# Performance work log

Measured on AMD Instinct MI355X. Metric: run time of the kernel, lower is better.

## Reference

```python
import jax, jax.numpy as jnp
import numpy as np

C = 256      # embed_dim
GROUP = 2    # conv groups
K = 3        # kernel/pool size
K2 = K * K
OG = 8       # offset groups (hard-coded in Similarity_cal)
NEX = 3      # exemplars per image (out_conv expects group*3*4 channels)


def conv2d(x, w, b, pad):
    y = jax.lax.conv_general_dilated(x, w, (1, 1), [(pad, pad), (pad, pad)],
                                     dimension_numbers=("NCHW", "OIHW", "NCHW"))
    return y + b[None, :, None, None]


def ln_c(x, g, b, eps=1e-5):
    # LayerNorm over the channel axis of NCHW (torch permutes to NHWC, LN, permute back)
    mu = x.mean(axis=1, keepdims=True)
    var = ((x - mu) ** 2).mean(axis=1, keepdims=True)
    return (x - mu) / jnp.sqrt(var + eps) * g[None, :, None, None] + b[None, :, None, None]


def bilinear_gather(img, py, px):
    # img [Cg,H,W]; py,px [K2,H,W] -> samples [Cg,K2,H,W], zero outside borders
    Cg, H, W = img.shape
    y0f = jnp.floor(py); x0f = jnp.floor(px)
    wy = py - y0f; wx = px - x0f
    y0 = y0f.astype(jnp.int32); x0 = x0f.astype(jnp.int32)
    flat = img.reshape(Cg, H * W)

    def corner(yy, xx, w):
        valid = (yy >= 0) & (yy < H) & (xx >= 0) & (xx < W)
        idx = jnp.clip(yy, 0, H - 1) * W + jnp.clip(xx, 0, W - 1)
        v = jnp.take(flat, idx.reshape(-1), axis=1).reshape(Cg, K2, H, W)
        return v * (w * valid)[None]

    return (corner(y0, x0, (1 - wy) * (1 - wx)) + corner(y0, x0 + 1, (1 - wy) * wx)
            + corner(y0 + 1, x0, wy * (1 - wx)) + corner(y0 + 1, x0 + 1, wy * wx))


def deform_conv(x, offset, mask, weight, dilation):
    # x [C,H,W]; offset [2*OG*K2,H,W]; mask [OG*K2,H,W] (softmaxed); weight [NEX*GROUP, C//GROUP, K, K]
    Cc, H, W = x.shape
    pad = (K - 1) * dilation // 2
    off = offset.reshape(OG, K2, 2, H, W)  # (dy, dx) per offset-group / tap
    kk = jnp.arange(K, dtype=x.dtype)
    ky = jnp.repeat(kk, K) * dilation - pad  # [K2]
    kx = jnp.tile(kk, K) * dilation - pad
    ii = jnp.arange(H, dtype=x.dtype)
    jj = jnp.arange(W, dtype=x.dtype)
    py = ii[None, None, :, None] + ky[None, :, None, None] + off[:, :, 0]  # [OG,K2,H,W]
    px = jj[None, None, None, :] + kx[None, :, None, None] + off[:, :, 1]
    xg = x.reshape(OG, Cc // OG, H, W)
    samp = jax.vmap(bilinear_gather)(xg, py, px)              # [OG,Cg,K2,H,W]
    samp = samp * mask.reshape(OG, 1, K2, H, W)               # modulation
    samp = samp.reshape(GROUP, Cc // GROUP, K2, H, W)
    wR = weight.reshape(NEX * GROUP, Cc // GROUP, K2)
    gidx = jnp.arange(NEX * GROUP) // NEX                     # out-channel -> conv group
    return jnp.einsum("rck,rckhw->rhw", wR, samp[gidx])       # [NEX*GROUP,H,W]


def forward(querys_feat, supports_feat, in_w, in_b, ln_g, ln_b, out_w, out_b,
            offw1, offb1, mskw1, mskb1, offw2, offb2, mskw2, mskb2,
            offw4, offb4, mskw4, mskb4):
    B = querys_feat.shape[0]
    q = ln_c(conv2d(querys_feat, in_w, in_b, 0), ln_g, ln_b)                 # [B,C,H,W]
    s = supports_feat.reshape(B * NEX, C, K, K)
    s = ln_c(conv2d(s, in_w, in_b, 0), ln_g, ln_b).reshape(B, NEX, C, K, K)

    def offs(wo, bo, wm, bm):
        o = conv2d(q, wo, bo, (K - 1) // 2)
        m = jax.nn.softmax(conv2d(q, wm, bm, (K - 1) // 2), axis=1)  # softmax over all OG*K2 channels
        return o, m

    o1, m1 = offs(offw1, offb1, mskw1, mskb1)
    o2, m2 = offs(offw2, offb2, mskw2, mskb2)
    o4, m4 = offs(offw4, offb4, mskw4, mskb4)

    def per_sample(qi, si, o1i, m1i, o2i, m2i, o4i, m4i):
        w = si.reshape(NEX * GROUP, C // GROUP, K, K)         # dynamic per-exemplar kernels
        pooled = si.max(axis=(2, 3)).reshape(NEX * GROUP, C // GROUP)
        gidx = jnp.arange(NEX * GROUP) // NEX
        qg = qi.reshape(GROUP, C // GROUP, *qi.shape[1:])
        sim0 = jnp.einsum("rc,rchw->rhw", pooled, qg[gidx])   # grouped 1x1 conv branch
        d1 = deform_conv(qi, o1i, m1i, w, 1)
        d2 = deform_conv(qi, o2i, m2i, w, 2)
        d4 = deform_conv(qi, o4i, m4i, w, 4)
        return jnp.concatenate([sim0, d1, d2, d4], axis=0)    # [GROUP*3*4, H, W]

    sim = jax.vmap(per_sample)(q, s, o1, m1, o2, m2, o4, m4)
    return conv2d(sim, out_w, out_b, 0)                        # [B,C,H,W]


def setup_inputs() -> dict:
    key = jax.random.key(0)
    ks = jax.random.split(key, 20)
    B, H, W = 2, 96, 96
    inp = {
        "querys_feat": jax.random.normal(ks[0], (B, C, H, W), jnp.float32),
        "supports_feat": jax.random.normal(ks[1], (B, NEX, C, K, K), jnp.float32),
        "in_w": jax.random.normal(ks[2], (C, C, 1, 1), jnp.float32) / 16.0,
        "in_b": jax.random.normal(ks[3], (C,), jnp.float32) * 0.02,
        "ln_g": jnp.ones((C,), jnp.float32),
        "ln_b": jnp.zeros((C,), jnp.float32),
        "out_w": jax.random.normal(ks[4], (C, GROUP * 3 * 4, 1, 1), jnp.float32) * 0.2,
        "out_b": jax.random.normal(ks[5], (C,), jnp.float32) * 0.02,
    }
    i = 6
    for d in (1, 2, 4):
        inp[f"offw{d}"] = jax.random.normal(ks[i], (2 * OG * K2, C, K, K), jnp.float32) * 0.01; i += 1
        inp[f"offb{d}"] = jax.random.normal(ks[i], (2 * OG * K2,), jnp.float32) * 0.1; i += 1
        inp[f"mskw{d}"] = jax.random.normal(ks[i], (OG * K2, C, K, K), jnp.float32) * 0.02; i += 1
        inp[f"mskb{d}"] = jax.random.normal(ks[i], (OG * K2,), jnp.float32) * 0.1; i += 1
    return inp


def reference(querys_feat, supports_feat, in_w, in_b, ln_g, ln_b, out_w, out_b,
              offw1, offb1, mskw1, mskb1, offw2, offb2, mskw2, mskb2,
              offw4, offb4, mskw4, mskb4):
    return forward(querys_feat, supports_feat, in_w, in_b, ln_g, ln_b, out_w, out_b,
                   offw1, offb1, mskw1, mskb1, offw2, offb2, mskw2, mskb2,
                   offw4, offb4, mskw4, mskb4)
```

## Files before the change

kernel.cpp:

```cpp
#include <hip/hip_runtime.h>
#include <hip/hip_bf16.h>
#include <math.h>

#define HH 96
#define WWID 96
#define HW 9216
#define CC 256
#define BB 2
#define PROW 104
#define PCOL 128
#define PPX (PROW * PCOL)

typedef float f32x4 __attribute__((ext_vector_type(4)));
typedef _Float16 f16x8 __attribute__((ext_vector_type(8)));
typedef _Float16 h2v __attribute__((ext_vector_type(2)));

__device__ inline unsigned int pack2h(float a, float b) {
  unsigned short ua = __builtin_bit_cast(unsigned short, (_Float16)a);
  unsigned short ub = __builtin_bit_cast(unsigned short, (_Float16)b);
  return (unsigned int)ua | ((unsigned int)ub << 16);
}

#if defined(__has_builtin)
#if __has_builtin(__builtin_amdgcn_fdot2)
#define FDOT2(a, b, c) __builtin_amdgcn_fdot2((a), (b), (c), false)
#endif
#endif
#ifndef FDOT2
#define FDOT2(a, b, c) ((c) + (float)(a).x * (float)(b).x + (float)(a).y * (float)(b).y)
#endif

__device__ inline void gload_lds16(const void* g, void* l) {
  __builtin_amdgcn_global_load_lds(
      (const __attribute__((address_space(1))) void*)g,
      (__attribute__((address_space(3))) void*)l, 16, 0, 0);
}

__global__ void k_transpose_w(const float* __restrict__ in_w, float* __restrict__ wT) {
  int k = blockIdx.x, c = threadIdx.x;
  wT[k * CC + c] = in_w[c * CC + k];
}

__global__ void k_packw(const float* __restrict__ ow1, const float* __restrict__ ob1,
                        const float* __restrict__ mw1, const float* __restrict__ mb1,
                        const float* __restrict__ ow2, const float* __restrict__ ob2,
                        const float* __restrict__ mw2, const float* __restrict__ mb2,
                        const float* __restrict__ ow4, const float* __restrict__ ob4,
                        const float* __restrict__ mw4, const float* __restrict__ mb4,
                        _Float16* __restrict__ Whf, float* __restrict__ Ball) {
  int idx = blockIdx.x * 256 + threadIdx.x;
  if (idx >= 3 * 256 * 2304) return;
  int d = idx / (256 * 2304);
  int rem = idx - d * 256 * 2304;
  int co = rem / 2304;
  int k = rem - co * 2304;
  int j = k >> 8, ci = k & 255;
  const float* ow = d == 0 ? ow1 : (d == 1 ? ow2 : ow4);
  const float* mw = d == 0 ? mw1 : (d == 1 ? mw2 : mw4);
  float v = 0.f;
  if (co < 144) v = ow[co * 2304 + ci * 9 + j];
  else if (co < 216) v = mw[(co - 144) * 2304 + ci * 9 + j];
  Whf[idx] = (_Float16)v;
  if (idx < 768) {
    int dd = idx >> 8, cc = idx & 255;
    const float* obv = dd == 0 ? ob1 : (dd == 1 ? ob2 : ob4);
    const float* mbv = dd == 0 ? mb1 : (dd == 1 ? mb2 : mb4);
    float bv = 0.f;
    if (cc < 144) bv = obv[cc];
    else if (cc < 216) bv = mbv[cc - 144];
    Ball[idx] = bv;
  }
}

__global__ void k_conv1_ln_q(const float* __restrict__ qin, const float* __restrict__ wT,
                             const float* __restrict__ in_b, const float* __restrict__ ln_g,
                             const float* __restrict__ ln_b, float* __restrict__ q_hwc,
                             _Float16* __restrict__ qpad) {
  int bx = blockIdx.x;
  int b = bx / 288;
  int hw0 = (bx % 288) * 32;
  int t = threadIdx.x;
  int lane = t & 63;
  int wv_id = t >> 6;
  __shared__ float xs[32 * 260];
  const float* qb = qin + (size_t)b * CC * HW;
  #pragma unroll
  for (int i = 0; i < 32; ++i) {
    int idx = t + i * 256;
    int p = idx & 31;
    int k = idx >> 5;
    xs[p * 260 + k] = qb[k * HW + hw0 + p];
  }
  __syncthreads();
  float acc[8][4];
  #pragma unroll
  for (int p = 0; p < 8; ++p) { acc[p][0]=0.f; acc[p][1]=0.f; acc[p][2]=0.f; acc[p][3]=0.f; }
  const float4* wT4 = (const float4*)wT;
  int p0 = wv_id * 8;
  for (int k = 0; k < 256; k += 4) {
    float4 w0 = wT4[(k + 0) * 64 + lane];
    float4 w1 = wT4[(k + 1) * 64 + lane];
    float4 w2 = wT4[(k + 2) * 64 + lane];
    float4 w3 = wT4[(k + 3) * 64 + lane];
    #pragma unroll
    for (int p = 0; p < 8; ++p) {
      float4 xv = *(const float4*)&xs[(p0 + p) * 260 + k];
      acc[p][0] += w0.x * xv.x + w1.x * xv.y + w2.x * xv.z + w3.x * xv.w;
      acc[p][1] += w0.y * xv.x + w1.y * xv.y + w2.y * xv.z + w3.y * xv.w;
      acc[p][2] += w0.z * xv.x + w1.z * xv.y + w2.z * xv.z + w3.z * xv.w;
      acc[p][3] += w0.w * xv.x + w1.w * xv.y + w2.w * xv.z + w3.w * xv.w;
    }
  }
  float4 bb = ((const float4*)in_b)[lane];
  float4 g4 = ((const float4*)ln_g)[lane];
  float4 b4 = ((const float4*)ln_b)[lane];
  #pragma unroll
  for (int p = 0; p < 8; ++p) {
    float y0 = acc[p][0] + bb.x, y1 = acc[p][1] + bb.y;
    float y2 = acc[p][2] + bb.z, y3 = acc[p][3] + bb.w;
    float s1 = y0 + y1 + y2 + y3;
    float s2 = y0*y0 + y1*y1 + y2*y2 + y3*y3;
    #pragma unroll
    for (int off = 32; off; off >>= 1) { s1 += __shfl_xor(s1, off); s2 += __shfl_xor(s2, off); }
    float mu = s1 * (1.f / 256.f);
    float rstd = rsqrtf(s2 * (1.f / 256.f) - mu * mu + 1e-5f);
    float4 o;
    o.x = (y0 - mu) * rstd * g4.x + b4.x;
    o.y = (y1 - mu) * rstd * g4.y + b4.y;
    o.z = (y2 - mu) * rstd * g4.z + b4.z;
    o.w = (y3 - mu) * rstd * g4.w + b4.w;
    int hw = hw0 + p0 + p;
    ((float4*)q_hwc)[((size_t)b * HW + hw) * 64 + lane] = o;
    int hh = hw / 96, ww = hw - hh * 96;
    int ppx = (hh + 4) * PCOL + ww + 4;
    struct alignas(8) h4 { _Float16 h[4]; };
    h4 oh;
    oh.h[0] = (_Float16)o.x; oh.h[1] = (_Float16)o.y;
    oh.h[2] = (_Float16)o.z; oh.h[3] = (_Float16)o.w;
    *(h4*)(qpad + ((size_t)b * PPX + ppx) * CC + lane * 4) = oh;
  }
}

__global__ void k_conv1_ln_s(const float* __restrict__ sup, const float* __restrict__ wT,
                             const float* __restrict__ in_b, const float* __restrict__ ln_g,
                             const float* __restrict__ ln_b, float* __restrict__ s_ln,
                             float* __restrict__ pooled) {
  int img = blockIdx.x;
  int t = threadIdx.x;
  __shared__ float xs[2304];
  __shared__ float red1[256], red2[256];
  #pragma unroll
  for (int p = 0; p < 9; ++p) xs[t * 9 + p] = sup[(size_t)img * 2304 + t * 9 + p];
  __syncthreads();
  float acc[9];
  #pragma unroll
  for (int p = 0; p < 9; ++p) acc[p] = 0.f;
  for (int k = 0; k < 256; ++k) {
    float wv = wT[k * CC + t];
    #pragma unroll
    for (int p = 0; p < 9; ++p) acc[p] += wv * xs[k * 9 + p];
  }
  float bias = in_b[t];
  #pragma unroll
  for (int p = 0; p < 9; ++p) acc[p] += bias;
  float g = ln_g[t], be = ln_b[t];
  float vals[9];
  #pragma unroll
  for (int p = 0; p < 9; ++p) {
    red1[t] = acc[p]; red2[t] = acc[p] * acc[p];
    __syncthreads();
    for (int s = 128; s > 0; s >>= 1) {
      if (t < s) { red1[t] += red1[t + s]; red2[t] += red2[t + s]; }
      __syncthreads();
    }
    float mu = red1[0] * (1.f / 256.f);
    float var = red2[0] * (1.f / 256.f) - mu * mu;
    float rstd = rsqrtf(var + 1e-5f);
    vals[p] = (acc[p] - mu) * rstd * g + be;
    __syncthreads();
  }
  #pragma unroll
  for (int p = 0; p < 9; ++p) s_ln[(size_t)img * 2304 + t * 9 + p] = vals[p];
  float mx = vals[0];
  #pragma unroll
  for (int p = 1; p < 9; ++p) mx = fmaxf(mx, vals[p]);
  int b = img / 3, e = img % 3;
  pooled[((size_t)b * 6 + e * 2 + (t >> 7)) * 128 + (t & 127)] = mx;
}


#define BAR() __builtin_amdgcn_s_barrier()
#define SCHEDB() __builtin_amdgcn_sched_barrier(0)
#define VMCNT(N) asm volatile("s_waitcnt vmcnt(" #N ")" ::: "memory")

#define MMA_ONE(M, N, S, QM, QN) \
  acc[(QM)*4+(M)][(QN)*2+(N)] = __builtin_amdgcn_mfma_f32_16x16x32_f16( \
      af[M][S], bf[(QN)*2+(N)][S], acc[(QM)*4+(M)][(QN)*2+(N)], 0, 0, 0);

#define MMA_Q(QM, QN) { \
  __builtin_amdgcn_s_setprio(1); \
  MMA_ONE(0,0,0,QM,QN) MMA_ONE(1,0,0,QM,QN) MMA_ONE(2,0,0,QM,QN) MMA_ONE(3,0,0,QM,QN) \
  MMA_ONE(0,1,0,QM,QN) MMA_ONE(1,1,0,QM,QN) MMA_ONE(2,1,0,QM,QN) MMA_ONE(3,1,0,QM,QN) \
  MMA_ONE(0,0,1,QM,QN) MMA_ONE(1,0,1,QM,QN) MMA_ONE(2,0,1,QM,QN) MMA_ONE(3,0,1,QM,QN) \
  MMA_ONE(0,1,1,QM,QN) MMA_ONE(1,1,1,QM,QN) MMA_ONE(2,1,1,QM,QN) MMA_ONE(3,1,1,QM,QN) \
  __builtin_amdgcn_s_setprio(0); }

#define LDA(BUF, QM) { \
  const char* p_ = smemB + (BUF) * 65536 + (wm * 128 + (QM) * 64 + l15) * 128; \
  af[0][0] = *(const f16x8*)(p_ + 0*2048 + rc0); af[0][1] = *(const f16x8*)(p_ + 0*2048 + rc1); \
  af[1][0] = *(const f16x8*)(p_ + 1*2048 + rc0); af[1][1] = *(const f16x8*)(p_ + 1*2048 + rc1); \
  af[2][0] = *(const f16x8*)(p_ + 2*2048 + rc0); af[2][1] = *(const f16x8*)(p_ + 2*2048 + rc1); \
  af[3][0] = *(const f16x8*)(p_ + 3*2048 + rc0); af[3][1] = *(const f16x8*)(p_ + 3*2048 + rc1); }

#define LDB(BUF, QN) { \
  const char* p_ = smemB + (BUF) * 65536 + 32768 + (wn * 64 + (QN) * 32 + l15) * 128; \
  bf[(QN)*2+0][0] = *(const f16x8*)(p_ + 0*2048 + rc0); bf[(QN)*2+0][1] = *(const f16x8*)(p_ + 0*2048 + rc1); \
  bf[(QN)*2+1][0] = *(const f16x8*)(p_ + 1*2048 + rc0); bf[(QN)*2+1][1] = *(const f16x8*)(p_ + 1*2048 + rc1); }

#define STAGEA(TILE, Q) { \
  gload_lds16(aBase + (size_t)((Q) * 64) * 2304 + (TILE) * 64, \
              smemB + ((TILE) & 1) * 65536 + (((Q) * 64 + wv * 8) * 128)); \
  gload_lds16(aBase + (size_t)(128 + (Q) * 64) * 2304 + (TILE) * 64, \
              smemB + ((TILE) & 1) * 65536 + ((128 + (Q) * 64 + wv * 8) * 128)); }

#define STAGEB(TILE, Q, PPX0, PPX1) { \
  int j_ = (TILE) >> 2; \
  int offp_ = (j_ / 3 - 1) * PCOL + (j_ % 3) - 1; \
  int cb_ = ((TILE) & 3) * 64; \
  int rs_ = (wv >> 2) * 64 + (Q) * 32 + (wv & 3) * 8; \
  gload_lds16(bBase + (size_t)((PPX0) + offp_) * CC + cb_, \
              smemB + ((TILE) & 1) * 65536 + 32768 + (rs_ * 128)); \
  gload_lds16(bBase + (size_t)((PPX1) + offp_) * CC + cb_, \
              smemB + ((TILE) & 1) * 65536 + 32768 + ((128 + rs_) * 128)); }

__global__ void __launch_bounds__(512) k_conv3_mfma8(
    const _Float16* __restrict__ qpad, const _Float16* __restrict__ Whf,
    const float* __restrict__ Ball, unsigned int* __restrict__ taprec) {
  int nb = blockIdx.x;
  int z = blockIdx.y;
  int d = z >> 1, b = z & 1;
  int t = threadIdx.x;
  int lane = t & 63, wv = t >> 6;
  int wm = wv >> 2, wn = wv & 3;
  int quad = lane >> 4, l15 = lane & 15;
  int l8 = lane >> 3, c7 = lane & 7;

  __shared__ _Float16 __attribute__((aligned(16))) smem[65536];
  char* smemB = (char*)smem;

  const _Float16* Wd = Whf + (size_t)d * 256 * 2304;
  const _Float16* qb = qpad + (size_t)b * PPX * CC;

  int scol = ((c7 ^ l8) << 3);
  int rc0 = ((quad ^ (l15 & 7)) << 4);
  int rc1 = (((4 | quad) ^ (l15 & 7)) << 4);

  const _Float16* aBase = Wd + (size_t)(wv * 8 + l8) * 2304 + scol;
  const _Float16* bBase = qb + scol;

  int ppx00, ppx01, ppx10, ppx11;
  {
    int rbase = (wv >> 2) * 64 + (wv & 3) * 8 + l8;
    int px, hh, ww;
    px = nb * 256 + rbase;             hh = px / 96; ww = px - hh * 96; ppx00 = (hh + 4) * PCOL + ww + 4;
    px = nb * 256 + 128 + rbase;       hh = px / 96; ww = px - hh * 96; ppx01 = (hh + 4) * PCOL + ww + 4;
    px = nb * 256 + 32 + rbase;        hh = px / 96; ww = px - hh * 96; ppx10 = (hh + 4) * PCOL + ww + 4;
    px = nb * 256 + 160 + rbase;       hh = px / 96; ww = px - hh * 96; ppx11 = (hh + 4) * PCOL + ww + 4;
  }

  f32x4 acc[8][4];
  #pragma unroll
  for (int i = 0; i < 8; ++i)
    #pragma unroll
    for (int j = 0; j < 4; ++j) acc[i][j] = (f32x4){0.f, 0.f, 0.f, 0.f};

  f16x8 af[4][2], bf[4][2];

  STAGEA(0, 0);
  STAGEB(0, 1, ppx10, ppx11);
  STAGEA(0, 1);
  STAGEB(0, 0, ppx00, ppx01);
  STAGEA(1, 0);
  STAGEB(1, 1, ppx10, ppx11);
  VMCNT(4);
  BAR();
  SCHEDB();

  #pragma unroll 1
  for (int ii = 0; ii < 17; ++ii) {
    int ta = 2 * ii + 1, tb = 2 * ii + 2, tc = 2 * ii + 3;
    LDA(0, 0) LDB(0, 0)
    STAGEA(ta, 1);
    BAR(); MMA_Q(0, 0); BAR();
    LDB(0, 1)
    STAGEB(ta, 0, ppx00, ppx01);
    BAR(); MMA_Q(0, 1); BAR();
    LDA(0, 1)
    STAGEA(tb, 0);
    BAR(); MMA_Q(1, 1); BAR();
    STAGEB(tb, 1, ppx10, ppx11);
    VMCNT(4);
    BAR(); SCHEDB(); MMA_Q(1, 0); BAR();
    LDA(1, 0) LDB(1, 0)
    STAGEA(tb, 1);
    BAR(); MMA_Q(0, 0); BAR();
    LDB(1, 1)
    STAGEB(tb, 0, ppx00, ppx01);
    BAR(); MMA_Q(0, 1); BAR();
    LDA(1, 1)
    STAGEA(tc, 0);
    BAR(); MMA_Q(1, 1); BAR();
    STAGEB(tc, 1, ppx10, ppx11);
    VMCNT(4);
    BAR(); SCHEDB(); MMA_Q(1, 0); BAR();
  }

  LDA(0, 0) LDB(0, 0)
  STAGEA(35, 1);
  BAR(); MMA_Q(0, 0); BAR();
  LDB(0, 1)
  STAGEB(35, 0, ppx00, ppx01);
  BAR(); MMA_Q(0, 1); BAR();
  LDA(0, 1)
  BAR(); MMA_Q(1, 1); BAR();
  VMCNT(0);
  BAR(); SCHEDB(); MMA_Q(1, 0); BAR();
  LDA(1, 0) LDB(1, 0)
  BAR(); MMA_Q(0, 0); BAR();
  LDB(1, 1)
  BAR(); MMA_Q(0, 1); BAR();
  LDA(1, 1)
  BAR(); MMA_Q(1, 1); BAR();
  MMA_Q(1, 0);

  BAR();
  float* cs = (float*)smemB;
  const float* Bd = Ball + d * 256;
  unsigned int* tzo = taprec + (size_t)z * 72 * HW * 3;
  int sub = t & 7;
  int pxq = t >> 3;
  int dil = 1 << d;

  #pragma unroll 1
  for (int H = 0; H < 2; ++H) {
    if ((wn >> 1) == H) {
      #pragma unroll
      for (int mi = 0; mi < 8; ++mi) {
        int c2 = wm * 128 + mi * 16 + quad * 4;
        if (c2 < 216) {
          float4 bq = *(const float4*)(Bd + c2);
          #pragma unroll
          for (int ni = 0; ni < 4; ++ni) {
            int pl = (wn & 1) * 64 + ni * 16 + l15;
            f32x4 v = acc[mi][ni];
            float* cp = &cs[pl * 225 + c2];
            cp[0] = v[0] + bq.x; cp[1] = v[1] + bq.y;
            cp[2] = v[2] + bq.z; cp[3] = v[3] + bq.w;
          }
        }
      }
    }
    BAR();
    #pragma unroll 1
    for (int p = 0; p < 2; ++p) {
      int pl = p * 64 + pxq;
      int px = nb * 256 + H * 128 + pl;
      const float* cr = &cs[pl * 225];
      float lg[9];
      float mx = -1e30f;
      #pragma unroll
      for (int j = 0; j < 9; ++j) {
        lg[j] = cr[144 + sub + 8 * j];
        mx = fmaxf(mx, lg[j]);
      }
      mx = fmaxf(mx, __shfl_xor(mx, 1));
      mx = fmaxf(mx, __shfl_xor(mx, 2));
      mx = fmaxf(mx, __shfl_xor(mx, 4));
      float s = 0.f;
      #pragma unroll
      for (int j = 0; j < 9; ++j) s += __expf(lg[j] - mx);
      s += __shfl_xor(s, 1);
      s += __shfl_xor(s, 2);
      s += __shfl_xor(s, 4);
      float rinv = 1.f / s;
      int h = px / WWID, w = px - h * WWID;
      int k = sub;
      #pragma unroll
      for (int j = 0; j < 9; ++j) {
        int tk = sub + 8 * j;
        float dy = cr[tk * 2 + 0];
        float dx = cr[tk * 2 + 1];
        float m = __expf(lg[j] - mx) * rinv;
        float py = (float)(h + (k / 3) * dil - dil) + dy;
        float pxx = (float)(w + (k % 3) * dil - dil) + dx;
        float y0f = floorf(py), x0f = floorf(pxx);
        int y0 = (int)y0f, x0 = (int)x0f;
        float wy = py - y0f, wx = pxx - x0f;
        bool vy0 = (unsigned)y0 < 96u, vy1 = (unsigned)(y0 + 1) < 96u;
        bool vx0 = (unsigned)x0 < 96u, vx1 = (unsigned)(x0 + 1) < 96u;
        float w00 = (vy0 && vx0) ? (1.f - wy) * (1.f - wx) * m : 0.f;
        float w01 = (vy0 && vx1) ? (1.f - wy) * wx * m : 0.f;
        float w10 = (vy1 && vx0) ? wy * (1.f - wx) * m : 0.f;
        float w11 = (vy1 && vx1) ? wy * wx * m : 0.f;
        int iy = min(max(y0 + 4, 0), 102);
        int ix = min(max(x0 + 4, 0), 126);
        unsigned int* r = tzo + ((size_t)tk * HW + px) * 3;
        r[0] = pack2h(w00, w01);
        r[1] = pack2h(w10, w11);
        r[2] = (unsigned int)(iy * PCOL + ix);
        k += 8; if (k >= 9) k -= 9;
      }
    }
    BAR();
  }
}

__global__ void k_sim0(const float* __restrict__ qt, const float* __restrict__ pooled,
                       float* __restrict__ sim) {
  int b = blockIdx.z, h = blockIdx.y, seg = blockIdx.x;
  int t = threadIdx.x;
  int pxl = t >> 5, lane = t & 31;
  int wcol = seg * 8 + pxl;
  int hw = h * WWID + wcol;
  __shared__ float plds[768];
  for (int i = t; i < 768; i += 256) plds[i] = pooled[(size_t)b * 768 + i];
  __syncthreads();
  const float* qtb = qt + (size_t)b * HW * CC;
  float acc[6] = {0.f, 0.f, 0.f, 0.f, 0.f, 0.f};
  #pragma unroll
  for (int m = 0; m < 8; ++m) {
    int cfull = m * 32 + lane;
    float qv = qtb[(size_t)hw * CC + cfull];
    if (m < 4) {
      int cp = cfull;
      acc[0] += plds[0 * 128 + cp] * qv;
      acc[1] += plds[1 * 128 + cp] * qv;
      acc[2] += plds[2 * 128 + cp] * qv;
    } else {
      int cp = cfull - 128;
      acc[3] += plds[3 * 128 + cp] * qv;
      acc[4] += plds[4 * 128 + cp] * qv;
      acc[5] += plds[5 * 128 + cp] * qv;
    }
  }
  #pragma unroll
  for (int r = 0; r < 6; ++r) {
    float v = acc[r];
    #pragma unroll
    for (int off = 16; off; off >>= 1) v += __shfl_down(v, off, 32);
    if (lane == 0) sim[((size_t)b * 24 + r) * HW + hw] = v;
  }
}

#define DO_P(U0, U1, IDX, P) { \
  h2v u0_ = __builtin_bit_cast(h2v, (U0)); \
  h2v u1_ = __builtin_bit_cast(h2v, (U1)); \
  const h2v* b0_ = qc + (size_t)(IDX) * 128; \
  h2v q00_ = b0_[0], q01_ = b0_[128]; \
  h2v q10_ = b0_[16384], q11_ = b0_[16384 + 128]; \
  h2v s_ = q00_ * (h2v){u0_.x, u0_.x} + q01_ * (h2v){u0_.y, u0_.y} \
         + q10_ * (h2v){u1_.x, u1_.x} + q11_ * (h2v){u1_.y, u1_.y}; \
  acc[P][0] = FDOT2(wr0, s_, acc[P][0]); \
  acc[P][1] = FDOT2(wr1, s_, acc[P][1]); \
  acc[P][2] = FDOT2(wr2, s_, acc[P][2]); }

__global__ void __launch_bounds__(256) k_deform(
    const _Float16* __restrict__ qpad, const unsigned int* __restrict__ taprec,
    const float* __restrict__ s_ln, float* __restrict__ sim) {
  int bid = blockIdx.x;
  int slab = bid & 7;
  int j = bid >> 3;
  int z = j / 72;
  int rem = j - z * 72;
  int yhalf = rem / 36;
  int segin = rem - yhalf * 36;
  int seg = slab * 36 + segin;
  int d_idx = z >> 1, b = z & 1;
  int t = threadIdx.x;
  int g = t >> 5, lane = t & 31;
  int half16 = lane >> 4, l16 = lane & 15;
  __shared__ _Float16 wh[9 * 384];
  __shared__ unsigned int rlds[36 * 96];
  int px0 = seg * 32;
  int tkbase = yhalf * 36;
  const unsigned int* tz = taprec + (size_t)z * 72 * HW * 3;
  for (int i2 = t; i2 < 3456; i2 += 256) {
    int c = i2 / 9, k = i2 % 9;
    wh[k * 384 + c] = (_Float16)s_ln[(size_t)b * 6912 + yhalf * 3456 + i2];
  }
  for (int i2 = t; i2 < 3456; i2 += 256) {
    int tko = i2 / 96, dw = i2 - tko * 96;
    rlds[i2] = tz[((size_t)(tkbase + tko) * HW + px0) * 3 + dw];
  }
  __syncthreads();
  int pg = g * 4;
  int pxb = px0 + pg;
  const unsigned int* whd = (const unsigned int*)wh;
  const _Float16* qb = qpad + (size_t)b * PPX * CC;

  float acc[4][3];
  #pragma unroll
  for (int p = 0; p < 4; ++p)
    #pragma unroll
    for (int r = 0; r < 3; ++r) acc[p][r] = 0.f;

  #pragma unroll 1
  for (int ogp = 0; ogp < 2; ++ogp) {
    int og = yhalf * 4 + ogp * 2 + half16;
    int qch = og * 32 + l16 * 2;
    int wcol = qch - yhalf * 128;
    int tko = (ogp * 2 + half16) * 9;
    const h2v* qc = (const h2v*)(qb + qch);
    #pragma unroll 3
    for (int k = 0; k < 9; ++k) {
      const unsigned int* rr = &rlds[(tko + k) * 96 + pg * 3];
      h2v wr0 = __builtin_bit_cast(h2v, whd[(k * 384 + 0 + wcol) >> 1]);
      h2v wr1 = __builtin_bit_cast(h2v, whd[(k * 384 + 128 + wcol) >> 1]);
      h2v wr2 = __builtin_bit_cast(h2v, whd[(k * 384 + 256 + wcol) >> 1]);
      DO_P(rr[0], rr[1], rr[2], 0)
      DO_P(rr[3], rr[4], rr[5], 1)
      DO_P(rr[6], rr[7], rr[8], 2)
      DO_P(rr[9], rr[10], rr[11], 3)
    }
  }

  #pragma unroll
  for (int p = 0; p < 4; ++p) {
    #pragma unroll
    for (int r = 0; r < 3; ++r) {
      float v = acc[p][r];
      #pragma unroll
      for (int off = 16; off; off >>= 1) v += __shfl_down(v, off, 32);
      if (lane == 0)
        sim[((size_t)b * 24 + 6 + 6 * d_idx + yhalf * 3 + r) * HW + pxb + p] = v;
    }
  }
}

__global__ void k_outconv(const float* __restrict__ sim, const float* __restrict__ out_w,
                          const float* __restrict__ out_b, float* __restrict__ out) {
  int hw = blockIdx.x * 256 + threadIdx.x;
  int co = blockIdx.y, b = blockIdx.z;
  const float* simb = sim + (size_t)b * 24 * HW;
  float a = out_b[co];
  #pragma unroll
  for (int r = 0; r < 24; ++r) a += out_w[co * 24 + r] * simb[(size_t)r * HW + hw];
  out[((size_t)b * CC + co) * HW + hw] = a;
}

extern "C" void kernel_launch(void* const* d_in, const int* in_sizes, int n_in,
                              void* d_out, int out_size, void* d_ws, size_t ws_size,
                              hipStream_t stream) {
  const float* querys = (const float*)d_in[0];
  const float* sup    = (const float*)d_in[1];
  const float* in_w   = (const float*)d_in[2];
  const float* in_b   = (const float*)d_in[3];
  const float* ln_g   = (const float*)d_in[4];
  const float* ln_b   = (const float*)d_in[5];
  const float* out_w  = (const float*)d_in[6];
  const float* out_b  = (const float*)d_in[7];
  const float* ow1 = (const float*)d_in[8];
  const float* ob1 = (const float*)d_in[9];
  const float* mw1 = (const float*)d_in[10];
  const float* mb1 = (const float*)d_in[11];
  const float* ow2 = (const float*)d_in[12];
  const float* ob2 = (const float*)d_in[13];
  const float* mw2 = (const float*)d_in[14];
  const float* mb2 = (const float*)d_in[15];
  const float* ow4 = (const float*)d_in[16];
  const float* ob4 = (const float*)d_in[17];
  const float* mw4 = (const float*)d_in[18];
  const float* mb4 = (const float*)d_in[19];
  float* out = (float*)d_out;

  float* ws_f   = (float*)d_ws;
  float* wT     = ws_f;
  _Float16* Whf = (_Float16*)(wT + 65536);
  float* Ball   = (float*)(Whf + 3 * 256 * 2304);
  float* q_hwc  = Ball + 1024;
  _Float16* qpad = (_Float16*)(q_hwc + (size_t)BB * HW * CC);
  float* s_ln   = (float*)(qpad + (size_t)BB * PPX * CC);
  float* pooled = s_ln + 13824;
  unsigned int* taprec = (unsigned int*)(pooled + 1536);
  float* sim    = (float*)(taprec + (size_t)6 * 72 * HW * 3);

  hipMemsetAsync(qpad, 0, (size_t)BB * PPX * CC * sizeof(_Float16), stream);
  k_transpose_w<<<dim3(256), dim3(256), 0, stream>>>(in_w, wT);
  k_packw<<<dim3((3 * 256 * 2304 + 255) / 256), dim3(256), 0, stream>>>(
      ow1, ob1, mw1, mb1, ow2, ob2, mw2, mb2, ow4, ob4, mw4, mb4, Whf, Ball);
  k_conv1_ln_q<<<dim3(576), dim3(256), 0, stream>>>(querys, wT, in_b, ln_g, ln_b, q_hwc, qpad);
  k_conv1_ln_s<<<dim3(6), dim3(256), 0, stream>>>(sup, wT, in_b, ln_g, ln_b, s_ln, pooled);
  k_conv3_mfma8<<<dim3(36, 6), dim3(512), 0, stream>>>(qpad, Whf, Ball, taprec);
  k_sim0<<<dim3(12, 96, BB), dim3(256), 0, stream>>>(q_hwc, pooled, sim);
  k_deform<<<dim3(3456), dim3(256), 0, stream>>>(qpad, taprec, s_ln, sim);
  k_outconv<<<dim3(36, 256, BB), dim3(256), 0, stream>>>(sim, out_w, out_b, out);
}
```

Measured before the change: 351.0 us.

## Fuse pooled-support similarity into query conv1+LN and merge weight prep kernels

Computes the sim0 dot products against pooled support features directly in the epilogue of the query 1x1 conv + LayerNorm kernel. This removes the fp32 q_hwc buffer write and reread and the separate k_sim0 launch. The transpose and weight-pack kernels are also merged into one launch. The support conv must now run before the query conv to supply pooled, and the epilogue gains extra shuffles and register use.

```diff
diff --git a/kernel.cpp b/kernel.cpp
--- a/kernel.cpp
+++ b/kernel.cpp
@@ -36,19 +36,21 @@
       (__attribute__((address_space(3))) void*)l, 16, 0, 0);
 }
 
-__global__ void k_transpose_w(const float* __restrict__ in_w, float* __restrict__ wT) {
-  int k = blockIdx.x, c = threadIdx.x;
-  wT[k * CC + c] = in_w[c * CC + k];
-}
-
-__global__ void k_packw(const float* __restrict__ ow1, const float* __restrict__ ob1,
-                        const float* __restrict__ mw1, const float* __restrict__ mb1,
-                        const float* __restrict__ ow2, const float* __restrict__ ob2,
-                        const float* __restrict__ mw2, const float* __restrict__ mb2,
-                        const float* __restrict__ ow4, const float* __restrict__ ob4,
-                        const float* __restrict__ mw4, const float* __restrict__ mb4,
-                        _Float16* __restrict__ Whf, float* __restrict__ Ball) {
-  int idx = blockIdx.x * 256 + threadIdx.x;
+__global__ void k_prep(const float* __restrict__ in_w, float* __restrict__ wT,
+                       const float* __restrict__ ow1, const float* __restrict__ ob1,
+                       const float* __restrict__ mw1, const float* __restrict__ mb1,
+                       const float* __restrict__ ow2, const float* __restrict__ ob2,
+                       const float* __restrict__ mw2, const float* __restrict__ mb2,
+                       const float* __restrict__ ow4, const float* __restrict__ ob4,
+                       const float* __restrict__ mw4, const float* __restrict__ mb4,
+                       _Float16* __restrict__ Whf, float* __restrict__ Ball) {
+  int bx = blockIdx.x;
+  int t = threadIdx.x;
+  if (bx < 256) {
+    wT[bx * CC + t] = in_w[t * CC + bx];
+    return;
+  }
+  int idx = (bx - 256) * 256 + t;
   if (idx >= 3 * 256 * 2304) return;
   int d = idx / (256 * 2304);
   int rem = idx - d * 256 * 2304;
@@ -74,8 +76,8 @@
 
 __global__ void k_conv1_ln_q(const float* __restrict__ qin, const float* __restrict__ wT,
                              const float* __restrict__ in_b, const float* __restrict__ ln_g,
-                             const float* __restrict__ ln_b, float* __restrict__ q_hwc,
-                             _Float16* __restrict__ qpad) {
+                             const float* __restrict__ ln_b, const float* __restrict__ pooled,
+                             _Float16* __restrict__ qpad, float* __restrict__ sim) {
   int bx = blockIdx.x;
   int b = bx / 288;
   int hw0 = (bx % 288) * 32;
@@ -114,6 +116,12 @@
   float4 bb = ((const float4*)in_b)[lane];
   float4 g4 = ((const float4*)ln_g)[lane];
   float4 b4 = ((const float4*)ln_b)[lane];
+  int lg = lane >> 5;
+  int lc = lane & 31;
+  const float4* pp = (const float4*)(pooled + (size_t)b * 768 + (lg * 3) * 128);
+  float4 pr0 = pp[lc];
+  float4 pr1 = pp[32 + lc];
+  float4 pr2 = pp[64 + lc];
   #pragma unroll
   for (int p = 0; p < 8; ++p) {
     float y0 = acc[p][0] + bb.x, y1 = acc[p][1] + bb.y;
@@ -130,7 +138,6 @@
     o.z = (y2 - mu) * rstd * g4.z + b4.z;
     o.w = (y3 - mu) * rstd * g4.w + b4.w;
     int hw = hw0 + p0 + p;
-    ((float4*)q_hwc)[((size_t)b * HW + hw) * 64 + lane] = o;
     int hh = hw / 96, ww = hw - hh * 96;
     int ppx = (hh + 4) * PCOL + ww + 4;
     struct alignas(8) h4 { _Float16 h[4]; };
@@ -138,6 +145,21 @@
     oh.h[0] = (_Float16)o.x; oh.h[1] = (_Float16)o.y;
     oh.h[2] = (_Float16)o.z; oh.h[3] = (_Float16)o.w;
     *(h4*)(qpad + ((size_t)b * PPX + ppx) * CC + lane * 4) = oh;
+    float r0 = pr0.x * o.x + pr0.y * o.y + pr0.z * o.z + pr0.w * o.w;
+    float r1 = pr1.x * o.x + pr1.y * o.y + pr1.z * o.z + pr1.w * o.w;
+    float r2 = pr2.x * o.x + pr2.y * o.y + pr2.z * o.z + pr2.w * o.w;
+    #pragma unroll
+    for (int off = 16; off; off >>= 1) {
+      r0 += __shfl_xor(r0, off);
+      r1 += __shfl_xor(r1, off);
+      r2 += __shfl_xor(r2, off);
+    }
+    if (lc == 0) {
+      size_t base = ((size_t)b * 24 + lg * 3) * HW + hw;
+      sim[base] = r0;
+      sim[base + HW] = r1;
+      sim[base + 2 * HW] = r2;
+    }
   }
 }
 
@@ -415,43 +437,6 @@
   }
 }
 
-__global__ void k_sim0(const float* __restrict__ qt, const float* __restrict__ pooled,
-                       float* __restrict__ sim) {
-  int b = blockIdx.z, h = blockIdx.y, seg = blockIdx.x;
-  int t = threadIdx.x;
-  int pxl = t >> 5, lane = t & 31;
-  int wcol = seg * 8 + pxl;
-  int hw = h * WWID + wcol;
-  __shared__ float plds[768];
-  for (int i = t; i < 768; i += 256) plds[i] = pooled[(size_t)b * 768 + i];
-  __syncthreads();
-  const float* qtb = qt + (size_t)b * HW * CC;
-  float acc[6] = {0.f, 0.f, 0.f, 0.f, 0.f, 0.f};
-  #pragma unroll
-  for (int m = 0; m < 8; ++m) {
-    int cfull = m * 32 + lane;
-    float qv = qtb[(size_t)hw * CC + cfull];
-    if (m < 4) {
-      int cp = cfull;
-      acc[0] += plds[0 * 128 + cp] * qv;
-      acc[1] += plds[1 * 128 + cp] * qv;
-      acc[2] += plds[2 * 128 + cp] * qv;
-    } else {
-      int cp = cfull - 128;
-      acc[3] += plds[3 * 128 + cp] * qv;
-      acc[4] += plds[4 * 128 + cp] * qv;
-      acc[5] += plds[5 * 128 + cp] * qv;
-    }
-  }
-  #pragma unroll
-  for (int r = 0; r < 6; ++r) {
-    float v = acc[r];
-    #pragma unroll
-    for (int off = 16; off; off >>= 1) v += __shfl_down(v, off, 32);
-    if (lane == 0) sim[((size_t)b * 24 + r) * HW + hw] = v;
-  }
-}
-
 #define DO_P(U0, U1, IDX, P) { \
   h2v u0_ = __builtin_bit_cast(h2v, (U0)); \
   h2v u1_ = __builtin_bit_cast(h2v, (U1)); \
@@ -577,21 +562,18 @@
   float* wT     = ws_f;
   _Float16* Whf = (_Float16*)(wT + 65536);
   float* Ball   = (float*)(Whf + 3 * 256 * 2304);
-  float* q_hwc  = Ball + 1024;
-  _Float16* qpad = (_Float16*)(q_hwc + (size_t)BB * HW * CC);
+  _Float16* qpad = (_Float16*)(Ball + 1024);
   float* s_ln   = (float*)(qpad + (size_t)BB * PPX * CC);
   float* pooled = s_ln + 13824;
   unsigned int* taprec = (unsigned int*)(pooled + 1536);
   float* sim    = (float*)(taprec + (size_t)6 * 72 * HW * 3);
 
   hipMemsetAsync(qpad, 0, (size_t)BB * PPX * CC * sizeof(_Float16), stream);
-  k_transpose_w<<<dim3(256), dim3(256), 0, stream>>>(in_w, wT);
-  k_packw<<<dim3((3 * 256 * 2304 + 255) / 256), dim3(256), 0, stream>>>(
-      ow1, ob1, mw1, mb1, ow2, ob2, mw2, mb2, ow4, ob4, mw4, mb4, Whf, Ball);
-  k_conv1_ln_q<<<dim3(576), dim3(256), 0, stream>>>(querys, wT, in_b, ln_g, ln_b, q_hwc, qpad);
+  k_prep<<<dim3(256 + 6912), dim3(256), 0, stream>>>(
+      in_w, wT, ow1, ob1, mw1, mb1, ow2, ob2, mw2, mb2, ow4, ob4, mw4, mb4, Whf, Ball);
   k_conv1_ln_s<<<dim3(6), dim3(256), 0, stream>>>(sup, wT, in_b, ln_g, ln_b, s_ln, pooled);
+  k_conv1_ln_q<<<dim3(576), dim3(256), 0, stream>>>(querys, wT, in_b, ln_g, ln_b, pooled, qpad, sim);
   k_conv3_mfma8<<<dim3(36, 6), dim3(512), 0, stream>>>(qpad, Whf, Ball, taprec);
-  k_sim0<<<dim3(12, 96, BB), dim3(256), 0, stream>>>(q_hwc, pooled, sim);
   k_deform<<<dim3(3456), dim3(256), 0, stream>>>(qpad, taprec, s_ln, sim);
   k_outconv<<<dim3(36, 256, BB), dim3(256), 0, stream>>>(sim, out_w, out_b, out);
 }
```

New measurement: 350.9 us. No clear change (-0.1%).
